# Performance work log

Measured on AMD Instinct MI355X. Metric: run time of the kernel, lower is better.

The kernel has to match this reference:

```python
import jax, jax.numpy as jnp
import numpy as np

B, T = 4, 2048
H, NH, NKV, HD = 2048, 16, 4, 128
THETA = 10000.0
SCALE = HD ** -0.5


def setup_inputs() -> dict:
    key = jax.random.key(0)
    ks = jax.random.split(key, 9)
    s = lambda n: 1.0 / np.sqrt(n)
    return {
        "hidden_states": jax.random.normal(ks[0], (B, T, H), jnp.float32),
        "positions": jnp.tile(jnp.arange(T, dtype=jnp.int32)[None, :], (B, 1)),
        "wq": jax.random.normal(ks[1], (H, NH * HD), jnp.float32) * s(H),
        "bq": jax.random.normal(ks[2], (NH * HD,), jnp.float32) * 0.01,
        "wk": jax.random.normal(ks[3], (H, NKV * HD), jnp.float32) * s(H),
        "bk": jax.random.normal(ks[4], (NKV * HD,), jnp.float32) * 0.01,
        "wv": jax.random.normal(ks[5], (H, NKV * HD), jnp.float32) * s(H),
        "bv": jax.random.normal(ks[6], (NKV * HD,), jnp.float32) * 0.01,
        "wo": jax.random.normal(ks[7], (NH * HD, H), jnp.float32) * s(NH * HD),
    }


def _rope(x, pos):
    # Neox-style RoPE over full head_dim. x: [B,T,n,HD], pos: [B,T]
    half = HD // 2
    inv_freq = 1.0 / (THETA ** (jnp.arange(half, dtype=jnp.float32) / half))
    freqs = pos.astype(jnp.float32)[..., None] * inv_freq  # [B,T,half]
    cos = jnp.cos(freqs)[:, :, None, :]
    sin = jnp.sin(freqs)[:, :, None, :]
    x1, x2 = x[..., :half], x[..., half:]
    return jnp.concatenate([x1 * cos - x2 * sin, x2 * cos + x1 * sin], axis=-1)


def reference(hidden_states, wq, bq, wk, bk, wv, bv, wo, positions):
    q = (hidden_states @ wq + bq).reshape(B, T, NH, HD)
    k = (hidden_states @ wk + bk).reshape(B, T, NKV, HD)
    v = (hidden_states @ wv + bv).reshape(B, T, NKV, HD)
    q = _rope(q, positions)
    k = _rope(k, positions)
    # GQA: repeat kv heads to match query heads
    rep = NH // NKV
    k = jnp.repeat(k, rep, axis=2)
    v = jnp.repeat(v, rep, axis=2)
    q = q.transpose(0, 2, 1, 3)  # [B,NH,T,HD]
    k = k.transpose(0, 2, 1, 3)
    v = v.transpose(0, 2, 1, 3)
    scores = jnp.einsum('bhqd,bhkd->bhqk', q, k) * SCALE
    causal = jnp.tril(jnp.ones((T, T), dtype=jnp.bool_))
    scores = jnp.where(causal[None, None, :, :], scores, -jnp.inf)
    w = jax.nn.softmax(scores, axis=-1).astype(v.dtype)
    o = jnp.einsum('bhqk,bhkd->bhqd', w, v)
    o = o.transpose(0, 2, 1, 3).reshape(B, T, NH * HD)
    return o @ wo
```

## Files before the change

kernel.cpp:

```cpp
#include <hip/hip_runtime.h>
#include <hip/hip_bf16.h>

#define TSEQ 2048
#define BATCH 4
#define NH 16
#define NKV 4
#define HD 128
#define NQKV 3072
#define SCALE_ 0.08838834764831845f

typedef __bf16 bf16x8 __attribute__((ext_vector_type(8)));
typedef float f32x4 __attribute__((ext_vector_type(4)));

__device__ __forceinline__ unsigned short f2bf(float f) {
    union { float f; unsigned u; } v; v.f = f;
    unsigned r = v.u + 0x7fffu + ((v.u >> 16) & 1u);
    return (unsigned short)(r >> 16);
}
__device__ __forceinline__ float bf2f(unsigned short b) {
    union { unsigned u; float f; } v; v.u = ((unsigned)b) << 16; return v.f;
}

__global__ __launch_bounds__(256) void xconv(const float* __restrict__ in,
                                             unsigned short* __restrict__ out) {
    const size_t i = (size_t)blockIdx.x * 256 + threadIdx.x;
    const float4 v = ((const float4*)in)[i];
    union { unsigned short u[4]; int2 p; } o;
    o.u[0] = f2bf(v.x); o.u[1] = f2bf(v.y); o.u[2] = f2bf(v.z); o.u[3] = f2bf(v.w);
    ((int2*)out)[i] = o.p;
}

__global__ __launch_bounds__(256) void wtrans_kernel(const float* __restrict__ in,
                                                     unsigned short* __restrict__ out,
                                                     int inN, int K) {
    __shared__ unsigned short l[64][65];
    const int n0 = blockIdx.x * 64, k0 = blockIdx.y * 64;
    const int tid = threadIdx.x;
    const int r = tid >> 2, c0 = (tid & 3) * 16;
#pragma unroll
    for (int i = 0; i < 16; i += 4) {
        float4 v = *(const float4*)&in[(size_t)(k0 + r) * inN + n0 + c0 + i];
        l[c0 + i + 0][r] = f2bf(v.x);
        l[c0 + i + 1][r] = f2bf(v.y);
        l[c0 + i + 2][r] = f2bf(v.z);
        l[c0 + i + 3][r] = f2bf(v.w);
    }
    __syncthreads();
    unsigned short tmp[16];
#pragma unroll
    for (int i = 0; i < 16; ++i) tmp[i] = l[r][c0 + i];
    *(int4*)&out[(size_t)(n0 + r) * K + k0 + c0] = *(int4*)&tmp[0];
    *(int4*)&out[(size_t)(n0 + r) * K + k0 + c0 + 8] = *(int4*)&tmp[8];
}

__global__ __launch_bounds__(256) void bias_concat(const float* __restrict__ bq,
                                                   const float* __restrict__ bk,
                                                   const float* __restrict__ bv,
                                                   float* __restrict__ out) {
    int i = blockIdx.x * 256 + threadIdx.x;
    out[i] = (i < 2048) ? bq[i] : ((i < 2560) ? bk[i - 2048] : bv[i - 2560]);
}

template <bool BIAS, bool OUTBF16>
__global__ __launch_bounds__(256) void gemm_bt(const unsigned short* __restrict__ A,
                                               const unsigned short* __restrict__ Bt,
                                               const float* __restrict__ bias,
                                               void* __restrict__ Cout,
                                               int M, int N, int K) {
    __shared__ unsigned short lA[128 * 32];
    __shared__ unsigned short lB[128 * 32];
    const int tid = threadIdx.x;
    const int lane = tid & 63, wid = tid >> 6;
    const int wr = wid >> 1, wc = wid & 1;
    const int g = lane >> 4, lr = lane & 15;
    const int bm = blockIdx.x * 128, bn = blockIdx.y * 128;

    f32x4 acc[4][4];
#pragma unroll
    for (int i = 0; i < 4; ++i)
#pragma unroll
        for (int j = 0; j < 4; ++j) acc[i][j] = f32x4{0.f, 0.f, 0.f, 0.f};

    for (int k0 = 0; k0 < K; k0 += 32) {
#pragma unroll
        for (int c = 0; c < 2; ++c) {
            const int off = c * 256 + tid;
            const int row = off >> 2, colb = (off & 3) * 16;
            __builtin_amdgcn_global_load_lds(
                (const __attribute__((address_space(1))) unsigned int*)
                    ((const char*)(A + (size_t)(bm + row) * K + k0) + colb),
                (__attribute__((address_space(3))) unsigned int*)
                    ((char*)lA + (c * 256 + wid * 64) * 16),
                16, 0, 0);
            __builtin_amdgcn_global_load_lds(
                (const __attribute__((address_space(1))) unsigned int*)
                    ((const char*)(Bt + (size_t)(bn + row) * K + k0) + colb),
                (__attribute__((address_space(3))) unsigned int*)
                    ((char*)lB + (c * 256 + wid * 64) * 16),
                16, 0, 0);
        }
        __syncthreads();
        bf16x8 af[4], bfr[4];
#pragma unroll
        for (int i = 0; i < 4; ++i)
            af[i] = *(const bf16x8*)((const char*)lA + (wr * 64 + i * 16 + lr) * 64 + g * 16);
#pragma unroll
        for (int j = 0; j < 4; ++j)
            bfr[j] = *(const bf16x8*)((const char*)lB + (wc * 64 + j * 16 + lr) * 64 + g * 16);
#pragma unroll
        for (int i = 0; i < 4; ++i)
#pragma unroll
            for (int j = 0; j < 4; ++j)
                acc[i][j] = __builtin_amdgcn_mfma_f32_16x16x32_bf16(af[i], bfr[j], acc[i][j], 0, 0, 0);
        __syncthreads();
    }
#pragma unroll
    for (int i = 0; i < 4; ++i)
#pragma unroll
        for (int j = 0; j < 4; ++j)
#pragma unroll
            for (int ii = 0; ii < 4; ++ii) {
                const int r = bm + wr * 64 + i * 16 + g * 4 + ii;
                const int c = bn + wc * 64 + j * 16 + lr;
                float v = acc[i][j][ii];
                if (BIAS) v += bias[c];
                if (OUTBF16)
                    ((unsigned short*)Cout)[(size_t)r * N + c] = f2bf(v);
                else
                    ((float*)Cout)[(size_t)r * N + c] = v;
            }
}

__global__ __launch_bounds__(256) void rope_kernel(unsigned short* __restrict__ QKV,
                                                   const int* __restrict__ positions) {
    const int tid = threadIdx.x;
    const int i = tid & 63;
    const int bt = blockIdx.x * 4 + (tid >> 6);
    const int head = blockIdx.y;
    unsigned short* base =
        QKV + (size_t)bt * NQKV + (head < NH ? head * HD : 2048 + (head - NH) * HD);
    const float pos = (float)positions[bt];
    const float invf = __expf(-(float)i * (9.21034037198e0f / 64.0f));
    const float f = pos * invf;
    const float sc = (head < NH) ? SCALE_ : 1.0f;
    const float c = cosf(f) * sc, s = sinf(f) * sc;
    const float x1 = bf2f(base[i]);
    const float x2 = bf2f(base[i + 64]);
    base[i] = f2bf(x1 * c - x2 * s);
    base[i + 64] = f2bf(x2 * c + x1 * s);
}

__global__ __launch_bounds__(256) void vtrans_kernel(const unsigned short* __restrict__ QKV,
                                                     unsigned short* __restrict__ Vt) {
    __shared__ unsigned short l[16][128];
    const int tid = threadIdx.x;
    const int t0 = blockIdx.x * 16, kvh = blockIdx.y, b = blockIdx.z;
#pragma unroll
    for (int i = 0; i < 8; ++i) {
        const int t = (tid >> 7) + i * 2, d = tid & 127;
        l[t][d] = QKV[(size_t)(b * TSEQ + t0 + t) * NQKV + 2560 + kvh * HD + d];
    }
    __syncthreads();
    const int d = tid >> 1, th = (tid & 1) * 8;
    unsigned short tmp[8];
#pragma unroll
    for (int i = 0; i < 8; ++i) tmp[i] = l[th + i][d];
    *(int4*)&Vt[((size_t)(b * NKV + kvh) * HD + d) * TSEQ + t0 + th] = *(int4*)tmp;
}

__global__ __launch_bounds__(512) void attn_kernel(const unsigned short* __restrict__ QKV,
                                                   const unsigned short* __restrict__ Vt,
                                                   unsigned short* __restrict__ O) {
    __shared__ unsigned short lK[2][64 * HD];
    __shared__ unsigned short lV[2][HD * 64];
    __shared__ unsigned short lP[128 * 64];
    const int tid = threadIdx.x, lane = tid & 63, w = tid >> 6;
    const int g = lane >> 4, lr = lane & 15;
    const int pair = blockIdx.x;
    const int h = blockIdx.y, b = blockIdx.z;
    const int kvh = h >> 2;

    const unsigned short* kgbase = QKV + (size_t)(b * TSEQ) * NQKV + 2048 + kvh * HD;
    const unsigned short* vgbase = Vt + (size_t)(b * NKV + kvh) * HD * TSEQ;

    auto stage = [&](int buf, int k0) {
#pragma unroll
        for (int c = 0; c < 2; ++c) {
            const int soff = (c * 512 + tid) * 16;
            {
                const int row = soff >> 8;
                const int off = soff ^ ((row & 7) << 4);
                __builtin_amdgcn_global_load_lds(
                    (const __attribute__((address_space(1))) unsigned int*)
                        ((const char*)(kgbase + (size_t)(k0 + row) * NQKV) + (off & 255)),
                    (__attribute__((address_space(3))) unsigned int*)
                        ((char*)lK[buf] + (c * 512 + w * 64) * 16),
                    16, 0, 0);
            }
            {
                const int row = soff >> 7;
                const int off = soff ^ ((row & 7) << 4);
                __builtin_amdgcn_global_load_lds(
                    (const __attribute__((address_space(1))) unsigned int*)
                        ((const char*)(vgbase + (size_t)row * TSEQ + (size_t)k0) + (off & 127)),
                    (__attribute__((address_space(3))) unsigned int*)
                        ((char*)lV[buf] + (c * 512 + w * 64) * 16),
                    16, 0, 0);
            }
        }
    };

    int cur = 0;
#pragma unroll 1
    for (int ph = 0; ph < 2; ++ph) {
        const int q0 = (ph == 0 ? (15 - pair) : pair) * 128;

        bf16x8 qf[4];
        {
            const unsigned short* qp =
                QKV + (size_t)(b * TSEQ + q0 + 16 * w + lr) * NQKV + h * HD;
#pragma unroll
            for (int kk = 0; kk < 4; ++kk) qf[kk] = *(const bf16x8*)(qp + kk * 32 + g * 8);
        }
        f32x4 oacc[8];
#pragma unroll
        for (int i = 0; i < 8; ++i) oacc[i] = f32x4{0.f, 0.f, 0.f, 0.f};
        float mrow[4] = {-1e30f, -1e30f, -1e30f, -1e30f};
        float lrow[4] = {0.f, 0.f, 0.f, 0.f};

        stage(cur, 0);
        __syncthreads();

        const int klast = q0 + 64;
        for (int k0 = 0; k0 <= klast; k0 += 64) {
            const bool more = (k0 < klast);
            if (more) stage(cur ^ 1, k0 + 64);

            const char* kb = (const char*)lK[cur];
            const char* vb = (const char*)lV[cur];

            f32x4 s[4];
#pragma unroll
            for (int j = 0; j < 4; ++j) s[j] = f32x4{0.f, 0.f, 0.f, 0.f};
#pragma unroll
            for (int kk = 0; kk < 4; ++kk) {
#pragma unroll
                for (int j = 0; j < 4; ++j) {
                    const int row = j * 16 + lr;
                    const int boff = (row * 256 + kk * 64 + g * 16) ^ ((row & 7) << 4);
                    bf16x8 kf = *(const bf16x8*)(kb + boff);
                    s[j] = __builtin_amdgcn_mfma_f32_16x16x32_bf16(qf[kk], kf, s[j], 0, 0, 0);
                }
            }
            if (k0 + 63 > q0 + 16 * w) {
#pragma unroll
                for (int j = 0; j < 4; ++j)
#pragma unroll
                    for (int ii = 0; ii < 4; ++ii) {
                        const int kglob = k0 + j * 16 + lr;
                        const int qglob = q0 + 16 * w + 4 * g + ii;
                        if (kglob > qglob) s[j][ii] = -1e30f;
                    }
            }
            float mnew[4];
#pragma unroll
            for (int ii = 0; ii < 4; ++ii)
                mnew[ii] = fmaxf(fmaxf(s[0][ii], s[1][ii]), fmaxf(s[2][ii], s[3][ii]));
#pragma unroll
            for (int d = 1; d < 16; d <<= 1)
#pragma unroll
                for (int ii = 0; ii < 4; ++ii)
                    mnew[ii] = fmaxf(mnew[ii], __shfl_xor(mnew[ii], d, 64));
            bool need = false;
#pragma unroll
            for (int ii = 0; ii < 4; ++ii) need = need || (mnew[ii] > mrow[ii] + 8.0f);
            if (__any(need)) {
#pragma unroll
                for (int ii = 0; ii < 4; ++ii) {
                    const float mN = fmaxf(mrow[ii], mnew[ii]);
                    const float resc = __expf(mrow[ii] - mN);
                    mrow[ii] = mN;
                    lrow[ii] *= resc;
#pragma unroll
                    for (int nf = 0; nf < 8; ++nf) oacc[nf][ii] *= resc;
                }
            }
#pragma unroll
            for (int j = 0; j < 4; ++j)
#pragma unroll
                for (int ii = 0; ii < 4; ++ii) {
                    const float p = __expf(s[j][ii] - mrow[ii]);
                    lrow[ii] += p;
                    const int prow = 16 * w + 4 * g + ii;
                    const int boff = (prow * 128 + (j * 16 + lr) * 2) ^ ((prow & 7) << 4);
                    *(unsigned short*)((char*)lP + boff) = f2bf(p);
                }
#pragma unroll
            for (int kk = 0; kk < 2; ++kk) {
                const int arow = 16 * w + lr;
                const int aoff = (arow * 128 + kk * 64 + g * 16) ^ ((arow & 7) << 4);
                bf16x8 pf = *(const bf16x8*)((const char*)lP + aoff);
#pragma unroll
                for (int nf = 0; nf < 8; ++nf) {
                    const int vrow = nf * 16 + lr;
                    const int voff = (vrow * 128 + kk * 64 + g * 16) ^ ((vrow & 7) << 4);
                    bf16x8 vf = *(const bf16x8*)(vb + voff);
                    oacc[nf] = __builtin_amdgcn_mfma_f32_16x16x32_bf16(pf, vf, oacc[nf], 0, 0, 0);
                }
            }
            __syncthreads();
            cur ^= 1;
        }
#pragma unroll
        for (int d = 1; d < 16; d <<= 1)
#pragma unroll
            for (int ii = 0; ii < 4; ++ii) lrow[ii] += __shfl_xor(lrow[ii], d, 64);
#pragma unroll
        for (int nf = 0; nf < 8; ++nf)
#pragma unroll
            for (int ii = 0; ii < 4; ++ii) {
                const int qrow = q0 + 16 * w + 4 * g + ii;
                const int col = h * HD + nf * 16 + lr;
                O[(size_t)(b * TSEQ + qrow) * (NH * HD) + col] = f2bf(oacc[nf][ii] / lrow[ii]);
            }
    }
}

extern "C" void kernel_launch(void* const* d_in, const int* in_sizes, int n_in,
                              void* d_out, int out_size, void* d_ws, size_t ws_size,
                              hipStream_t stream) {
    const float* hs = (const float*)d_in[0];
    const int* positions = (const int*)d_in[1];
    const float* wq = (const float*)d_in[2];
    const float* bq = (const float*)d_in[3];
    const float* wk = (const float*)d_in[4];
    const float* bk = (const float*)d_in[5];
    const float* wv = (const float*)d_in[6];
    const float* bv = (const float*)d_in[7];
    const float* wo = (const float*)d_in[8];
    float* out = (float*)d_out;

    const size_t SZ_XB = (size_t)8192 * 2048 * 2;
    const size_t SZ_WQKV = (size_t)3072 * 2048 * 2;
    const size_t SZ_WOT = (size_t)2048 * 2048 * 2;
    const size_t SZ_BIAS = 3072 * 4;
    const size_t SZ_QKV = (size_t)8192 * 3072 * 2;
    const size_t SZ_VT = (size_t)BATCH * NKV * HD * TSEQ * 2;
    const size_t SZ_OB = (size_t)8192 * 2048 * 2;

    char* ws = (char*)d_ws;
    unsigned short *Xb, *WqkvT, *WoT, *QKVb, *Vtb, *Ob;
    float* bqkv;
    const size_t need = SZ_XB + SZ_WQKV + SZ_WOT + SZ_BIAS + SZ_QKV + SZ_VT + SZ_OB + 2048;
    size_t off = 0;
    auto take = [&](size_t n) { char* p = ws + off; off += (n + 255) & ~(size_t)255; return p; };
    if (ws_size >= need) {
        Xb = (unsigned short*)take(SZ_XB);
        WqkvT = (unsigned short*)take(SZ_WQKV);
        Vtb = (unsigned short*)take(SZ_VT);
        WoT = (unsigned short*)take(SZ_WOT);
        bqkv = (float*)take(SZ_BIAS);
        QKVb = (unsigned short*)take(SZ_QKV);
        Ob = (unsigned short*)take(SZ_OB);
    } else {
        char* od = (char*)d_out;
        Xb = (unsigned short*)od;
        WqkvT = (unsigned short*)(od + SZ_XB);
        Vtb = (unsigned short*)(od + SZ_XB + SZ_WQKV);
        WoT = (unsigned short*)take(SZ_WOT);
        bqkv = (float*)take(SZ_BIAS);
        QKVb = (unsigned short*)take(SZ_QKV);
        Ob = (unsigned short*)take(SZ_OB);
    }

    xconv<<<16384, 256, 0, stream>>>(hs, Xb);
    wtrans_kernel<<<dim3(32, 32), 256, 0, stream>>>(wq, WqkvT, 2048, 2048);
    wtrans_kernel<<<dim3(8, 32), 256, 0, stream>>>(wk, WqkvT + (size_t)2048 * 2048, 512, 2048);
    wtrans_kernel<<<dim3(8, 32), 256, 0, stream>>>(wv, WqkvT + (size_t)2560 * 2048, 512, 2048);
    wtrans_kernel<<<dim3(32, 32), 256, 0, stream>>>(wo, WoT, 2048, 2048);
    bias_concat<<<12, 256, 0, stream>>>(bq, bk, bv, bqkv);
    gemm_bt<true, true><<<dim3(64, 24), 256, 0, stream>>>(Xb, WqkvT, bqkv, QKVb, 8192, 3072, 2048);
    rope_kernel<<<dim3(2048, 20), 256, 0, stream>>>(QKVb, positions);
    vtrans_kernel<<<dim3(128, 4, 4), 256, 0, stream>>>(QKVb, Vtb);
    attn_kernel<<<dim3(8, 16, 4), 512, 0, stream>>>(QKVb, Vtb, Ob);
    gemm_bt<false, false><<<dim3(64, 16), 256, 0, stream>>>(Ob, WoT, nullptr, out, 8192, 2048, 2048);
}
```

Measured before the change: 474.4 us.

## Replace 128x128 GEMM with double-buffered 256x256 swizzled-LDS GEMM

Both projection GEMMs move to a new 512-thread kernel with 256x256 output tiles and a K-step of 64. Loads are double-buffered in LDS so the next tile's global-to-LDS copy overlaps the current MFMA work, and an XOR chunk swizzle avoids LDS bank conflicts. Workgroups are remapped across the 8 XCDs for L2 locality, and bias is loaded once per column. The cost is much larger LDS use (128KB per block) and higher register pressure from 32 accumulator tiles, which limits occupancy to one block per CU. With only 384 and 256 blocks, the grids are small relative to the CU count.

Result: faster. 436.2 us (-8.0%).

```diff
diff --git a/kernel.cpp b/kernel.cpp
--- a/kernel.cpp
+++ b/kernel.cpp
@@ -62,73 +62,100 @@
 }
 
 template <bool BIAS, bool OUTBF16>
-__global__ __launch_bounds__(256) void gemm_bt(const unsigned short* __restrict__ A,
+__global__ __launch_bounds__(512) void gemm256(const unsigned short* __restrict__ A,
                                                const unsigned short* __restrict__ Bt,
                                                const float* __restrict__ bias,
                                                void* __restrict__ Cout,
-                                               int M, int N, int K) {
-    __shared__ unsigned short lA[128 * 32];
-    __shared__ unsigned short lB[128 * 32];
-    const int tid = threadIdx.x;
-    const int lane = tid & 63, wid = tid >> 6;
-    const int wr = wid >> 1, wc = wid & 1;
+                                               int M, int N, int K, int mtiles) {
+    __shared__ unsigned short lA[2][256 * 64];
+    __shared__ unsigned short lB[2][256 * 64];
+    const int tid = threadIdx.x, lane = tid & 63, wid = tid >> 6;
+    const int wr = wid >> 2, wc = wid & 3;
     const int g = lane >> 4, lr = lane & 15;
-    const int bm = blockIdx.x * 128, bn = blockIdx.y * 128;
-
-    f32x4 acc[4][4];
-#pragma unroll
-    for (int i = 0; i < 4; ++i)
-#pragma unroll
-        for (int j = 0; j < 4; ++j) acc[i][j] = f32x4{0.f, 0.f, 0.f, 0.f};
-
-    for (int k0 = 0; k0 < K; k0 += 32) {
-#pragma unroll
-        for (int c = 0; c < 2; ++c) {
-            const int off = c * 256 + tid;
-            const int row = off >> 2, colb = (off & 3) * 16;
+    const int nwg = gridDim.x;
+    const int q = nwg >> 3;
+    const int wg = (blockIdx.x & 7) * q + (blockIdx.x >> 3);
+    const int bm = (wg % mtiles) * 256, bn = (wg / mtiles) * 256;
+
+    f32x4 acc[8][4];
+#pragma unroll
+    for (int m = 0; m < 8; ++m)
+#pragma unroll
+        for (int n = 0; n < 4; ++n) acc[m][n] = f32x4{0.f, 0.f, 0.f, 0.f};
+
+    auto stage = [&](int buf, int k0) {
+#pragma unroll
+        for (int c = 0; c < 4; ++c) {
+            const int soff = (c * 512 + tid) * 16;
+            const int row = soff >> 7;
+            const int chunk = ((soff >> 4) & 7) ^ (row & 7);
+            const unsigned lbase = (unsigned)(c * 512 + wid * 64) * 16;
             __builtin_amdgcn_global_load_lds(
                 (const __attribute__((address_space(1))) unsigned int*)
-                    ((const char*)(A + (size_t)(bm + row) * K + k0) + colb),
-                (__attribute__((address_space(3))) unsigned int*)
-                    ((char*)lA + (c * 256 + wid * 64) * 16),
+                    (A + (size_t)(bm + row) * K + k0 + chunk * 8),
+                (__attribute__((address_space(3))) unsigned int*)((char*)lA[buf] + lbase),
                 16, 0, 0);
             __builtin_amdgcn_global_load_lds(
                 (const __attribute__((address_space(1))) unsigned int*)
-                    ((const char*)(Bt + (size_t)(bn + row) * K + k0) + colb),
-                (__attribute__((address_space(3))) unsigned int*)
-                    ((char*)lB + (c * 256 + wid * 64) * 16),
+                    (Bt + (size_t)(bn + row) * K + k0 + chunk * 8),
+                (__attribute__((address_space(3))) unsigned int*)((char*)lB[buf] + lbase),
                 16, 0, 0);
         }
-        __syncthreads();
-        bf16x8 af[4], bfr[4];
-#pragma unroll
-        for (int i = 0; i < 4; ++i)
-            af[i] = *(const bf16x8*)((const char*)lA + (wr * 64 + i * 16 + lr) * 64 + g * 16);
-#pragma unroll
-        for (int j = 0; j < 4; ++j)
-            bfr[j] = *(const bf16x8*)((const char*)lB + (wc * 64 + j * 16 + lr) * 64 + g * 16);
-#pragma unroll
-        for (int i = 0; i < 4; ++i)
-#pragma unroll
-            for (int j = 0; j < 4; ++j)
-                acc[i][j] = __builtin_amdgcn_mfma_f32_16x16x32_bf16(af[i], bfr[j], acc[i][j], 0, 0, 0);
+    };
+
+    stage(0, 0);
+    __syncthreads();
+    const int NT = K >> 6;
+    for (int t = 0; t < NT; ++t) {
+        const int buf = t & 1;
+        if (t + 1 < NT) stage(buf ^ 1, (t + 1) << 6);
+        __builtin_amdgcn_sched_barrier(0);
+        const char* pa = (const char*)lA[buf];
+        const char* pb = (const char*)lB[buf];
+#pragma unroll
+        for (int kk = 0; kk < 2; ++kk) {
+            bf16x8 bfr[4];
+#pragma unroll
+            for (int n = 0; n < 4; ++n) {
+                const int row = wc * 64 + n * 16 + lr;
+                bfr[n] = *(const bf16x8*)(pb + row * 128 + ((((kk << 2) + g) ^ (row & 7)) << 4));
+            }
+#pragma unroll
+            for (int mh = 0; mh < 2; ++mh) {
+                bf16x8 af[4];
+#pragma unroll
+                for (int m = 0; m < 4; ++m) {
+                    const int row = wr * 128 + (mh * 4 + m) * 16 + lr;
+                    af[m] = *(const bf16x8*)(pa + row * 128 + ((((kk << 2) + g) ^ (row & 7)) << 4));
+                }
+                __builtin_amdgcn_s_setprio(1);
+#pragma unroll
+                for (int m = 0; m < 4; ++m)
+#pragma unroll
+                    for (int n = 0; n < 4; ++n)
+                        acc[mh * 4 + m][n] = __builtin_amdgcn_mfma_f32_16x16x32_bf16(
+                            af[m], bfr[n], acc[mh * 4 + m][n], 0, 0, 0);
+                __builtin_amdgcn_s_setprio(0);
+            }
+        }
         __syncthreads();
     }
 #pragma unroll
-    for (int i = 0; i < 4; ++i)
-#pragma unroll
-        for (int j = 0; j < 4; ++j)
+    for (int m = 0; m < 8; ++m)
+#pragma unroll
+        for (int n = 0; n < 4; ++n) {
+            const int col = bn + wc * 64 + n * 16 + lr;
+            const float bv = BIAS ? bias[col] : 0.f;
 #pragma unroll
             for (int ii = 0; ii < 4; ++ii) {
-                const int r = bm + wr * 64 + i * 16 + g * 4 + ii;
-                const int c = bn + wc * 64 + j * 16 + lr;
-                float v = acc[i][j][ii];
-                if (BIAS) v += bias[c];
+                const int r = bm + wr * 128 + m * 16 + g * 4 + ii;
+                const float v = acc[m][n][ii] + bv;
                 if (OUTBF16)
-                    ((unsigned short*)Cout)[(size_t)r * N + c] = f2bf(v);
+                    ((unsigned short*)Cout)[(size_t)r * N + col] = f2bf(v);
                 else
-                    ((float*)Cout)[(size_t)r * N + c] = v;
-            }
+                    ((float*)Cout)[(size_t)r * N + col] = v;
+            }
+        }
 }
 
 __global__ __launch_bounds__(256) void rope_kernel(unsigned short* __restrict__ QKV,
@@ -379,9 +406,9 @@
     wtrans_kernel<<<dim3(8, 32), 256, 0, stream>>>(wv, WqkvT + (size_t)2560 * 2048, 512, 2048);
     wtrans_kernel<<<dim3(32, 32), 256, 0, stream>>>(wo, WoT, 2048, 2048);
     bias_concat<<<12, 256, 0, stream>>>(bq, bk, bv, bqkv);
-    gemm_bt<true, true><<<dim3(64, 24), 256, 0, stream>>>(Xb, WqkvT, bqkv, QKVb, 8192, 3072, 2048);
+    gemm256<true, true><<<384, 512, 0, stream>>>(Xb, WqkvT, bqkv, QKVb, 8192, 3072, 2048, 32);
     rope_kernel<<<dim3(2048, 20), 256, 0, stream>>>(QKVb, positions);
     vtrans_kernel<<<dim3(128, 4, 4), 256, 0, stream>>>(QKVb, Vtb);
     attn_kernel<<<dim3(8, 16, 4), 512, 0, stream>>>(QKVb, Vtb, Ob);
-    gemm_bt<false, false><<<dim3(64, 16), 256, 0, stream>>>(Ob, WoT, nullptr, out, 8192, 2048, 2048);
-}
+    gemm256<false, false><<<256, 512, 0, stream>>>(Ob, WoT, nullptr, out, 8192, 2048, 2048, 32);
+}
```
